# Kernel optimization log

Measured on AMD Instinct MI355X. Metric: run time of the kernel, lower is better.

## Reference

```python
import jax, jax.numpy as jnp
import numpy as np

EMBED_DIM = 1024
NUM_HEADS = 16
HEAD_DIM = EMBED_DIM // NUM_HEADS
NEG = -1000000000.0


def setup_inputs() -> dict:
    key = jax.random.key(0)
    ks = jax.random.split(key, 13)
    B, S, D = 4, 2048, EMBED_DIM
    scale = 1.0 / np.sqrt(D)
    inp = {
        "query": jax.random.normal(ks[0], (B, S, D), jnp.float32),
        "key": jax.random.normal(ks[1], (B, S, D), jnp.float32),
        "value": jax.random.normal(ks[2], (B, S, D), jnp.float32),
        "mask": jax.random.randint(ks[3], (B, 1, 1, S), 0, 2, jnp.int32),
        "Wq": jax.random.normal(ks[4], (D, D), jnp.float32) * scale,
        "bq": jnp.zeros((D,), jnp.float32),
        "Wk": jax.random.normal(ks[5], (D, D), jnp.float32) * scale,
        "bk": jnp.zeros((D,), jnp.float32),
        "Wv": jax.random.normal(ks[6], (D, D), jnp.float32) * scale,
        "bv": jnp.zeros((D,), jnp.float32),
        "Wo": jax.random.normal(ks[7], (D, D), jnp.float32) * scale,
        "bo": jnp.zeros((D,), jnp.float32),
    }
    return inp


def _split_heads(x):
    B, S, D = x.shape
    return x.reshape(B, S, NUM_HEADS, HEAD_DIM).transpose(0, 2, 1, 3)  # [B,H,S,hd]


def reference(query, key, value, mask, Wq, bq, Wk, bk, Wv, bv, Wo, bo):
    B, S, D = query.shape
    Q = _split_heads(query @ Wq + bq)
    K = _split_heads(key @ Wk + bk)
    V = _split_heads(value @ Wv + bv)
    scores = jnp.einsum("bhqd,bhkd->bhqk", Q, K) / jnp.sqrt(jnp.float32(HEAD_DIM))
    scores = jnp.where(mask == 0, jnp.float32(NEG), scores)
    attn = jax.nn.softmax(scores, axis=-1)
    out = jnp.einsum("bhqk,bhkd->bhqd", attn, V)
    out = out.transpose(0, 2, 1, 3).reshape(B, S, D)
    return out @ Wo + bo
```

## Files before the change

### kernel.cpp

```cpp
#include <hip/hip_runtime.h>


#define SEQ   2048
#define EDIM  1024
#define NHEAD 16
#define HDIM  64
#define NBAT  4
#define MTOK  8192

typedef __attribute__((ext_vector_type(8))) __bf16 bf16x8;
typedef __attribute__((ext_vector_type(4))) __bf16 bf16x4;
typedef __attribute__((ext_vector_type(4))) float f32x4;
typedef __attribute__((ext_vector_type(16))) float f32x16;
typedef __attribute__((ext_vector_type(8))) unsigned short us8;
typedef unsigned short u16;

#define SCL   0.1803368801111244f
#define MADD_OK   (-12.0f)
#define MADD_MASK (-100000.0f)

__device__ __forceinline__ u16 bfbits(float f) {
    __bf16 h = (__bf16)f;
    return __builtin_bit_cast(u16, h);
}
__device__ __forceinline__ bf16x8 bc(us8 v) { return __builtin_bit_cast(bf16x8, v); }
__device__ __forceinline__ float exp2fast(float x) {
    float r;
    asm("v_exp_f32 %0, %1" : "=v"(r) : "v"(x));
    return r;
}

__global__ __launch_bounds__(256) void prep_kernel(const int* __restrict__ mask,
                                                   int* __restrict__ idxl,
                                                   int* __restrict__ cntp) {
    __shared__ int psum[257];
    const int b = blockIdx.x, t = threadIdx.x;
    const int* mp = mask + b * SEQ;
    int m8[8]; int s = 0;
#pragma unroll
    for (int i = 0; i < 8; ++i) { m8[i] = mp[t * 8 + i]; s += (m8[i] != 0); }
    psum[t + 1] = s;
    __syncthreads();
    if (t == 0) { psum[0] = 0; for (int i = 1; i <= 256; ++i) psum[i] += psum[i - 1]; }
    __syncthreads();
    int ex = psum[t];
#pragma unroll
    for (int i = 0; i < 8; ++i)
        if (m8[i] != 0) idxl[b * SEQ + (ex++)] = t * 8 + i;
    if (t == 0) cntp[b] = psum[256];
}

__global__ __launch_bounds__(256) void wtrans4_kernel(const float* __restrict__ W0,
                                                      const float* __restrict__ W1,
                                                      const float* __restrict__ W2,
                                                      const float* __restrict__ W3,
                                                      u16* __restrict__ WT) {
    __shared__ float tile[32][33];
    const int tx = threadIdx.x, ty = threadIdx.y;
    const int bx = blockIdx.x,  by = blockIdx.y, wz = blockIdx.z;
    const float* W = (wz == 0) ? W0 : (wz == 1) ? W1 : (wz == 2) ? W2 : W3;
    u16* O = WT + (size_t)wz * EDIM * EDIM;
#pragma unroll
    for (int i = 0; i < 4; ++i)
        tile[ty + i * 8][tx] = W[(size_t)(by * 32 + ty + i * 8) * EDIM + bx * 32 + tx];
    __syncthreads();
#pragma unroll
    for (int i = 0; i < 4; ++i) {
        int n = bx * 32 + ty + i * 8;
        int k = by * 32 + tx;
        O[(size_t)n * EDIM + k] = bfbits(tile[tx][ty + i * 8]);
    }
}

template <int MODE, bool ABF16, bool GATHER>
__global__ __launch_bounds__(256) void gemm_kernel(const void* __restrict__ Ap,
                                                   const u16* __restrict__ WT,
                                                   const float* __restrict__ bias,
                                                   void* __restrict__ outp,
                                                   const int* __restrict__ idxl,
                                                   const int* __restrict__ cntp) {
    const int bm = blockIdx.x, bn = blockIdx.y;
    int cn = 0;
    if constexpr (GATHER) {
        cn = cntp[bm >> 4];
        if (((bm & 15) * 128) >= cn) return;
    }

    __shared__ u16 As[128][56];
    __shared__ u16 Bs[128][56];

    const int tid  = threadIdx.x;
    const int lane = tid & 63, wave = tid >> 6;
    const int g    = lane >> 4, l15 = lane & 15;
    const int wrow = wave >> 1, wcol = wave & 1;
    const int tr   = tid >> 1, tk = (tid & 1) * 16;

    int arow;
    if constexpr (GATHER) {
        const int sloc = (bm & 15) * 128 + tr;
        const int gi = (sloc < cn) ? idxl[(bm >> 4) * SEQ + sloc] : 0;
        arow = (bm >> 4) * SEQ + gi;
    } else {
        arow = bm * 128 + tr;
    }

    f32x4 acc[4][4] = {};

    bf16x8 sa0, sa1, sb0, sb1;
    auto LOAD = [&](int k0) {
        if constexpr (ABF16) {
            const u16* A = (const u16*)Ap;
            const u16* p = A + (size_t)arow * EDIM + k0 + tk;
            sa0 = bc(*(const us8*)p);
            sa1 = bc(*(const us8*)(p + 8));
        } else {
            const float* A = (const float*)Ap;
            const float* p = A + (size_t)arow * EDIM + k0 + tk;
            f32x4 v0 = *(const f32x4*)p;
            f32x4 v1 = *(const f32x4*)(p + 4);
            f32x4 v2 = *(const f32x4*)(p + 8);
            f32x4 v3 = *(const f32x4*)(p + 12);
#pragma unroll
            for (int j = 0; j < 4; ++j) {
                sa0[j] = (__bf16)v0[j]; sa0[4 + j] = (__bf16)v1[j];
                sa1[j] = (__bf16)v2[j]; sa1[4 + j] = (__bf16)v3[j];
            }
        }
        const u16* q = WT + (size_t)(bn * 128 + tr) * EDIM + k0 + tk;
        sb0 = bc(*(const us8*)q);
        sb1 = bc(*(const us8*)(q + 8));
    };

    LOAD(0);
#pragma unroll 1
    for (int kt = 0; kt < EDIM / 32; ++kt) {
        __syncthreads();
        *(bf16x8*)&As[tr][tk]     = sa0;
        *(bf16x8*)&As[tr][tk + 8] = sa1;
        *(bf16x8*)&Bs[tr][tk]     = sb0;
        *(bf16x8*)&Bs[tr][tk + 8] = sb1;
        __syncthreads();
        if (kt < EDIM / 32 - 1) LOAD((kt + 1) * 32);

        bf16x8 af[4], bfr[4];
#pragma unroll
        for (int i = 0; i < 4; ++i)
            af[i] = bc(*(const us8*)&As[wrow * 64 + i * 16 + l15][g * 8]);
#pragma unroll
        for (int j = 0; j < 4; ++j)
            bfr[j] = bc(*(const us8*)&Bs[wcol * 64 + j * 16 + l15][g * 8]);
#pragma unroll
        for (int i = 0; i < 4; ++i)
#pragma unroll
            for (int j = 0; j < 4; ++j)
                acc[i][j] = __builtin_amdgcn_mfma_f32_16x16x32_bf16(af[i], bfr[j], acc[i][j], 0, 0, 0);
    }

#pragma unroll
    for (int i = 0; i < 4; ++i) {
#pragma unroll
        for (int j = 0; j < 4; ++j) {
            const int gm0 = bm * 128 + wrow * 64 + i * 16 + g * 4;
            const int gn  = bn * 128 + wcol * 64 + j * 16 + l15;
            const float bv = bias[gn];
#pragma unroll
            for (int r = 0; r < 4; ++r) {
                float val = acc[i][j][r] + bv;
                const int m = gm0 + r;
                if constexpr (GATHER) {
                    if ((m & 2047) >= cn) val = 0.f;
                }
                if constexpr (MODE == 2) {
                    ((float*)outp)[(size_t)m * EDIM + gn] = val;
                } else {
                    const int b = m >> 11, s = m & 2047;
                    const int h = gn >> 6, d = gn & 63;
                    u16* O = (u16*)outp;
                    if constexpr (MODE == 0)
                        O[((size_t)(b * NHEAD + h) << 17) + s * HDIM + d] = bfbits(val);
                    else
                        O[((size_t)(b * NHEAD + h) << 17) + d * SEQ + s] = bfbits(val);
                }
            }
        }
    }
}

__global__ __launch_bounds__(256) void attn_kernel(const u16* __restrict__ Q,
                                                   const u16* __restrict__ K,
                                                   const u16* __restrict__ VT,
                                                   const int* __restrict__ cntp,
                                                   u16* __restrict__ O) {
    __shared__ u16 Klds[2][64][64];
    __shared__ u16 Vlds[2][64][64];
    __shared__ float madd[SEQ];

    const int tid = threadIdx.x, lane = tid & 63, w = tid >> 6;
    const int h = lane >> 5, l31 = lane & 31;

    const int id  = blockIdx.x;
    const int bh  = (id & 7) * 8 + ((id >> 3) >> 4);
    const int qb  = (id >> 3) & 15;
    const int b   = bh >> 4, hd_ = bh & 15;

    const u16* Qp = Q + ((size_t)bh << 17);
    const u16* Kp = K + ((size_t)bh << 17);
    const u16* Vp = VT + ((size_t)bh << 17);
    const int q0w = qb * 128 + w * 32;

    const int cn  = cntp[b];
    const int ktc = (cn + 63) >> 6;

    for (int i = tid; i < ktc * 64; i += 256)
        madd[i] = (i < cn) ? MADD_OK : MADD_MASK;

    bf16x8 qf[4];
#pragma unroll
    for (int khd = 0; khd < 4; ++khd)
        qf[khd] = bc(*(const us8*)&Qp[(size_t)(q0w + l31) * HDIM + khd * 16 + h * 8]);

    const int b_  = l31 & 3, hp = (l31 >> 2) & 1, cc = l31 >> 3;
    const int piR = 16 * (cc & 1) + 8 * hp + 4 * (cc >> 1) + b_;
    const int swk = (piR & 3) ^ (((piR >> 3) & 3) << 1);
    const int swv = l31 & 7;

    const int sr = tid >> 2, cu = (tid & 3) * 16;
    const int ksw = ((sr & 3) ^ (((sr >> 3) & 3) << 1)) << 3;
    const int vsw = (sr & 7) << 3;
    const int kc0 = cu ^ ksw, kc1 = (cu + 8) ^ ksw;
    const int vc0 = cu ^ vsw, vc1 = (cu + 8) ^ vsw;

    f32x16 ot[2] = {};
    float lsum = 0.f;

    {
        us8 a0 = *(const us8*)&Kp[(size_t)sr * HDIM + cu];
        us8 a1 = *(const us8*)&Kp[(size_t)sr * HDIM + cu + 8];
        us8 a2 = *(const us8*)&Vp[(size_t)sr * SEQ + cu];
        us8 a3 = *(const us8*)&Vp[(size_t)sr * SEQ + cu + 8];
        *(us8*)&Klds[0][sr][kc0] = a0;
        *(us8*)&Klds[0][sr][kc1] = a1;
        *(us8*)&Vlds[0][sr][vc0] = a2;
        *(us8*)&Vlds[0][sr][vc1] = a3;
    }
    __syncthreads();

    for (int kt = 0; kt < ktc; ++kt) {
        const int cur = kt & 1;
        const int kbase = kt * 64;
        const bool more = (kt + 1) < ktc;

        us8 nk0, nk1, nv0, nv1;
        if (more) {
            const int nb = kbase + 64;
            nk0 = *(const us8*)&Kp[(size_t)(nb + sr) * HDIM + cu];
            nk1 = *(const us8*)&Kp[(size_t)(nb + sr) * HDIM + cu + 8];
            nv0 = *(const us8*)&Vp[(size_t)sr * SEQ + nb + cu];
            nv1 = *(const us8*)&Vp[(size_t)sr * SEQ + nb + cu + 8];
        }

        f32x16 st[2] = {};
        __builtin_amdgcn_s_setprio(1);
#pragma unroll
        for (int kb2 = 0; kb2 < 2; ++kb2) {
            const u16* Kr = &Klds[cur][kb2 * 32 + piR][0];
#pragma unroll
            for (int khd = 0; khd < 4; ++khd) {
                bf16x8 kf = bc(*(const us8*)&Kr[(khd * 16 + h * 8) ^ (swk << 3)]);
                st[kb2] = __builtin_amdgcn_mfma_f32_32x32x16_bf16(kf, qf[khd], st[kb2], 0, 0, 0);
            }
        }
        __builtin_amdgcn_s_setprio(0);

        float pv[2][16];
#pragma unroll
        for (int kb2 = 0; kb2 < 2; ++kb2) {
#pragma unroll
            for (int cp = 0; cp < 4; ++cp) {
                const f32x4 ma = *(const f32x4*)&madd[kbase + kb2 * 32 + 16 * (cp & 1) + 4 * (cp >> 1) + 8 * h];
#pragma unroll
                for (int j = 0; j < 4; ++j) {
                    const float pe = exp2fast(fmaf(st[kb2][cp * 4 + j], SCL, ma[j]));
                    pv[kb2][cp * 4 + j] = pe;
                    lsum += pe;
                }
            }
        }

        bf16x8 pf[4];
#pragma unroll
        for (int s = 0; s < 4; ++s) {
            const int kb2 = s >> 1, sel = (s & 1) * 4;
#pragma unroll
            for (int j = 0; j < 4; ++j) {
                pf[s][j]     = (__bf16)pv[kb2][sel + j];
                pf[s][4 + j] = (__bf16)pv[kb2][8 + sel + j];
            }
        }

        __builtin_amdgcn_s_setprio(1);
#pragma unroll
        for (int dblk = 0; dblk < 2; ++dblk) {
            const u16* Vr = &Vlds[cur][dblk * 32 + l31][0];
#pragma unroll
            for (int s = 0; s < 4; ++s) {
                bf16x8 vf = bc(*(const us8*)&Vr[(s * 16 + h * 8) ^ (swv << 3)]);
                ot[dblk] = __builtin_amdgcn_mfma_f32_32x32x16_bf16(vf, pf[s], ot[dblk], 0, 0, 0);
            }
        }
        __builtin_amdgcn_s_setprio(0);

        if (more) {
            *(us8*)&Klds[cur ^ 1][sr][kc0] = nk0;
            *(us8*)&Klds[cur ^ 1][sr][kc1] = nk1;
            *(us8*)&Vlds[cur ^ 1][sr][vc0] = nv0;
            *(us8*)&Vlds[cur ^ 1][sr][vc1] = nv1;
        }
        __syncthreads();
    }

    lsum += __shfl_xor(lsum, 32);
    const float inv = 1.f / lsum;

    const size_t row = (size_t)(b * SEQ + q0w + l31) * EDIM + hd_ * HDIM;
#pragma unroll
    for (int dblk = 0; dblk < 2; ++dblk) {
#pragma unroll
        for (int cp = 0; cp < 4; ++cp) {
            bf16x4 t;
#pragma unroll
            for (int j = 0; j < 4; ++j)
                t[j] = (__bf16)(ot[dblk][cp * 4 + j] * inv);
            *(bf16x4*)&O[row + dblk * 32 + 8 * cp + 4 * h] = t;
        }
    }
}

extern "C" void kernel_launch(void* const* d_in, const int* in_sizes, int n_in,
                              void* d_out, int out_size, void* d_ws, size_t ws_size,
                              hipStream_t stream) {
    const float* query = (const float*)d_in[0];
    const float* key   = (const float*)d_in[1];
    const float* value = (const float*)d_in[2];
    const int*   mask  = (const int*)d_in[3];
    const float* Wq = (const float*)d_in[4];  const float* bq = (const float*)d_in[5];
    const float* Wk = (const float*)d_in[6];  const float* bk = (const float*)d_in[7];
    const float* Wv = (const float*)d_in[8];  const float* bv = (const float*)d_in[9];
    const float* Wo = (const float*)d_in[10]; const float* bo = (const float*)d_in[11];

    char* ws = (char*)d_ws;
    const size_t WT_BYTES  = (size_t)EDIM * EDIM * 2;
    const size_t BUF_BYTES = (size_t)MTOK * EDIM * 2;
    u16* wtq   = (u16*)(ws);
    u16* wtk   = (u16*)(ws + WT_BYTES);
    u16* wtv   = (u16*)(ws + 2 * WT_BYTES);
    u16* wto   = (u16*)(ws + 3 * WT_BYTES);
    u16* Qbuf  = (u16*)(ws + 4 * WT_BYTES);
    u16* Kbuf  = (u16*)(ws + 4 * WT_BYTES + BUF_BYTES);
    u16* VTbuf = (u16*)(ws + 4 * WT_BYTES + 2 * BUF_BYTES);
    u16* Abuf  = (u16*)(ws + 4 * WT_BYTES + 3 * BUF_BYTES);
    int* idxl  = (int*)(ws + 4 * WT_BYTES + 4 * BUF_BYTES);
    int* cntp  = (int*)(ws + 4 * WT_BYTES + 4 * BUF_BYTES + (size_t)MTOK * 4);

    prep_kernel<<<NBAT, 256, 0, stream>>>(mask, idxl, cntp);

    dim3 tgrid(32, 32, 4), tblk(32, 8);
    wtrans4_kernel<<<tgrid, tblk, 0, stream>>>(Wq, Wk, Wv, Wo, wtq);

    dim3 ggrid(MTOK / 128, EDIM / 128);
    gemm_kernel<0, false, false><<<ggrid, 256, 0, stream>>>(query, wtq, bq, Qbuf, nullptr, nullptr);
    gemm_kernel<0, false, true ><<<ggrid, 256, 0, stream>>>(key,   wtk, bk, Kbuf, idxl, cntp);
    gemm_kernel<1, false, true ><<<ggrid, 256, 0, stream>>>(value, wtv, bv, VTbuf, idxl, cntp);

    attn_kernel<<<1024, 256, 0, stream>>>(Qbuf, Kbuf, VTbuf, cntp, Abuf);

    gemm_kernel<2, true, false><<<ggrid, 256, 0, stream>>>(Abuf, wto, bo, (float*)d_out, nullptr, nullptr);
}
```

Baseline: 205.8 us.

## Use direct global-to-LDS loads with double-buffered swizzled tiles in projection GEMMs

The GEMM kernel now stages A and B tiles straight from global memory into LDS with global_load_lds, double-buffers them, and drops one barrier per k-step. For fp32 activations the raw floats are staged and converted to bf16 when read from LDS, and an XOR swizzle replaces row padding to avoid bank conflicts. The goal is to overlap the next tile's loads with the MFMA work and remove register round-trips. The cost is that fp32 A tiles double their LDS footprint, and correctness depends on the swizzle matching the per-lane layout that global_load_lds writes.

```diff
diff --git a/kernel.cpp b/kernel.cpp
--- a/kernel.cpp
+++ b/kernel.cpp
@@ -28,6 +28,11 @@
     float r;
     asm("v_exp_f32 %0, %1" : "=v"(r) : "v"(x));
     return r;
+}
+__device__ __forceinline__ void glds16(const void* g, void* l) {
+    __builtin_amdgcn_global_load_lds(
+        (const __attribute__((address_space(1))) unsigned int*)g,
+        (__attribute__((address_space(3))) unsigned int*)l, 16, 0, 0);
 }
 
 __global__ __launch_bounds__(256) void prep_kernel(const int* __restrict__ mask,
@@ -72,7 +77,7 @@
     }
 }
 
-template <int MODE, bool ABF16, bool GATHER>
+template <int MODE, bool AFP32, bool GATHER>
 __global__ __launch_bounds__(256) void gemm_kernel(const void* __restrict__ Ap,
                                                    const u16* __restrict__ WT,
                                                    const float* __restrict__ bias,
@@ -86,74 +91,116 @@
         if (((bm & 15) * 128) >= cn) return;
     }
 
-    __shared__ u16 As[128][56];
-    __shared__ u16 Bs[128][56];
+    __shared__ __align__(16) char Asraw[2][128 * 32 * (AFP32 ? 4 : 2)];
+    __shared__ __align__(16) u16 Bs[2][128][32];
 
     const int tid  = threadIdx.x;
-    const int lane = tid & 63, wave = tid >> 6;
+    const int lane = tid & 63, w = tid >> 6;
     const int g    = lane >> 4, l15 = lane & 15;
-    const int wrow = wave >> 1, wcol = wave & 1;
-    const int tr   = tid >> 1, tk = (tid & 1) * 16;
-
-    int arow;
-    if constexpr (GATHER) {
-        const int sloc = (bm & 15) * 128 + tr;
-        const int gi = (sloc < cn) ? idxl[(bm >> 4) * SEQ + sloc] : 0;
-        arow = (bm >> 4) * SEQ + gi;
+    const int wrow = w >> 1, wcol = w & 1;
+
+    const char* pa[4];
+    if constexpr (AFP32) {
+        const float* A = (const float*)Ap;
+#pragma unroll
+        for (int t = 0; t < 4; ++t) {
+            const int rloc = w * 32 + t * 8 + (lane >> 3);
+            int arow;
+            if constexpr (GATHER) {
+                const int sloc = (bm & 15) * 128 + rloc;
+                const int gi = (sloc < cn) ? idxl[(bm >> 4) * SEQ + sloc] : 0;
+                arow = (bm >> 4) * SEQ + gi;
+            } else arow = bm * 128 + rloc;
+            const int scol = ((lane & 7) ^ (lane >> 3)) * 4;
+            pa[t] = (const char*)(A + (size_t)arow * EDIM + scol);
+        }
     } else {
-        arow = bm * 128 + tr;
-    }
+        const u16* A = (const u16*)Ap;
+#pragma unroll
+        for (int t = 0; t < 2; ++t) {
+            const int rloc = w * 32 + t * 16 + (lane >> 2);
+            const int arow = bm * 128 + rloc;
+            const int scol = ((lane & 3) ^ ((lane >> 3) & 3)) * 8;
+            pa[t] = (const char*)(A + (size_t)arow * EDIM + scol);
+        }
+    }
+    const char* pb[2];
+#pragma unroll
+    for (int t = 0; t < 2; ++t) {
+        const int rloc = w * 32 + t * 16 + (lane >> 2);
+        const int brow = bn * 128 + rloc;
+        const int scol = ((lane & 3) ^ ((lane >> 3) & 3)) * 8;
+        pb[t] = (const char*)(WT + (size_t)brow * EDIM + scol);
+    }
+
+    auto STAGE = [&](int buf, int ko) {
+        char* abase = &Asraw[buf][0] + w * (AFP32 ? 4096 : 2048);
+        if constexpr (AFP32) {
+#pragma unroll
+            for (int t = 0; t < 4; ++t)
+                glds16(pa[t] + (size_t)ko * 4, abase + t * 1024);
+        } else {
+#pragma unroll
+            for (int t = 0; t < 2; ++t)
+                glds16(pa[t] + (size_t)ko * 2, abase + t * 1024);
+        }
+        char* bbase = (char*)&Bs[buf][0][0] + w * 2048;
+#pragma unroll
+        for (int t = 0; t < 2; ++t)
+            glds16(pb[t] + (size_t)ko * 2, bbase + t * 1024);
+    };
 
     f32x4 acc[4][4] = {};
 
-    bf16x8 sa0, sa1, sb0, sb1;
-    auto LOAD = [&](int k0) {
-        if constexpr (ABF16) {
-            const u16* A = (const u16*)Ap;
-            const u16* p = A + (size_t)arow * EDIM + k0 + tk;
-            sa0 = bc(*(const us8*)p);
-            sa1 = bc(*(const us8*)(p + 8));
-        } else {
-            const float* A = (const float*)Ap;
-            const float* p = A + (size_t)arow * EDIM + k0 + tk;
-            f32x4 v0 = *(const f32x4*)p;
-            f32x4 v1 = *(const f32x4*)(p + 4);
-            f32x4 v2 = *(const f32x4*)(p + 8);
-            f32x4 v3 = *(const f32x4*)(p + 12);
-#pragma unroll
-            for (int j = 0; j < 4; ++j) {
-                sa0[j] = (__bf16)v0[j]; sa0[4 + j] = (__bf16)v1[j];
-                sa1[j] = (__bf16)v2[j]; sa1[4 + j] = (__bf16)v3[j];
-            }
-        }
-        const u16* q = WT + (size_t)(bn * 128 + tr) * EDIM + k0 + tk;
-        sb0 = bc(*(const us8*)q);
-        sb1 = bc(*(const us8*)(q + 8));
-    };
-
-    LOAD(0);
+    STAGE(0, 0);
+    __syncthreads();
+
+    int buf = 0;
 #pragma unroll 1
     for (int kt = 0; kt < EDIM / 32; ++kt) {
-        __syncthreads();
-        *(bf16x8*)&As[tr][tk]     = sa0;
-        *(bf16x8*)&As[tr][tk + 8] = sa1;
-        *(bf16x8*)&Bs[tr][tk]     = sb0;
-        *(bf16x8*)&Bs[tr][tk + 8] = sb1;
-        __syncthreads();
-        if (kt < EDIM / 32 - 1) LOAD((kt + 1) * 32);
+        if (kt < EDIM / 32 - 1) STAGE(buf ^ 1, (kt + 1) * 32);
 
         bf16x8 af[4], bfr[4];
-#pragma unroll
-        for (int i = 0; i < 4; ++i)
-            af[i] = bc(*(const us8*)&As[wrow * 64 + i * 16 + l15][g * 8]);
-#pragma unroll
-        for (int j = 0; j < 4; ++j)
-            bfr[j] = bc(*(const us8*)&Bs[wcol * 64 + j * 16 + l15][g * 8]);
+        if constexpr (AFP32) {
+            const float* As = (const float*)&Asraw[buf][0];
+            const int x = l15 & 7;
+#pragma unroll
+            for (int i = 0; i < 4; ++i) {
+                const int row = wrow * 64 + i * 16 + l15;
+                f32x4 u0 = *(const f32x4*)(As + row * 32 + (((2 * g)     ^ x) * 4));
+                f32x4 u1 = *(const f32x4*)(As + row * 32 + (((2 * g + 1) ^ x) * 4));
+#pragma unroll
+                for (int j = 0; j < 4; ++j) {
+                    af[i][j]     = (__bf16)u0[j];
+                    af[i][4 + j] = (__bf16)u1[j];
+                }
+            }
+        } else {
+            const u16* As = (const u16*)&Asraw[buf][0];
+            const int x = (l15 >> 1) & 3;
+#pragma unroll
+            for (int i = 0; i < 4; ++i) {
+                const int row = wrow * 64 + i * 16 + l15;
+                af[i] = bc(*(const us8*)(As + row * 32 + ((g ^ x) * 8)));
+            }
+        }
+        {
+            const int x = (l15 >> 1) & 3;
+#pragma unroll
+            for (int j = 0; j < 4; ++j) {
+                const int row = wcol * 64 + j * 16 + l15;
+                bfr[j] = bc(*(const us8*)((const u16*)&Bs[buf][0][0] + row * 32 + ((g ^ x) * 8)));
+            }
+        }
+
 #pragma unroll
         for (int i = 0; i < 4; ++i)
 #pragma unroll
             for (int j = 0; j < 4; ++j)
                 acc[i][j] = __builtin_amdgcn_mfma_f32_16x16x32_bf16(af[i], bfr[j], acc[i][j], 0, 0, 0);
+
+        __syncthreads();
+        buf ^= 1;
     }
 
 #pragma unroll
@@ -368,11 +415,11 @@
     wtrans4_kernel<<<tgrid, tblk, 0, stream>>>(Wq, Wk, Wv, Wo, wtq);
 
     dim3 ggrid(MTOK / 128, EDIM / 128);
-    gemm_kernel<0, false, false><<<ggrid, 256, 0, stream>>>(query, wtq, bq, Qbuf, nullptr, nullptr);
-    gemm_kernel<0, false, true ><<<ggrid, 256, 0, stream>>>(key,   wtk, bk, Kbuf, idxl, cntp);
-    gemm_kernel<1, false, true ><<<ggrid, 256, 0, stream>>>(value, wtv, bv, VTbuf, idxl, cntp);
+    gemm_kernel<0, true,  false><<<ggrid, 256, 0, stream>>>(query, wtq, bq, Qbuf, nullptr, nullptr);
+    gemm_kernel<0, true,  true ><<<ggrid, 256, 0, stream>>>(key,   wtk, bk, Kbuf, idxl, cntp);
+    gemm_kernel<1, true,  true ><<<ggrid, 256, 0, stream>>>(value, wtv, bv, VTbuf, idxl, cntp);
 
     attn_kernel<<<1024, 256, 0, stream>>>(Qbuf, Kbuf, VTbuf, cntp, Abuf);
 
-    gemm_kernel<2, true, false><<<ggrid, 256, 0, stream>>>(Abuf, wto, bo, (float*)d_out, nullptr, nullptr);
-}
+    gemm_kernel<2, false, false><<<ggrid, 256, 0, stream>>>(Abuf, wto, bo, (float*)d_out, nullptr, nullptr);
+}
```

Measured after the change: 199.9 us. -2.9%, faster.
